# Kernel optimization log

Hardware: AMD Instinct MI355X
Metric: run time of the kernel (lower is better)

Reference implementation:

```python
import jax, jax.numpy as jnp
import numpy as np

TEMPERATURE = 0.1
EPS = 1e-8


def setup_inputs() -> dict:
    key = jax.random.key(0)
    k1, k2 = jax.random.split(key)
    N, D = 4096, 512
    features = jax.random.normal(k1, (N, D), dtype=jnp.float32)
    labels = jax.random.randint(k2, (N,), 0, 100, dtype=jnp.int64)
    return {"features": features, "labels": labels}


def reference(features, labels):
    # FFT along feature dim -> complex (N, D)
    cf = jnp.fft.fft(features)
    N = cf.shape[0]

    # All-pairs complex dot product expressed as a GEMM:
    # Re(sum_d u_d * conj(v_d)) for every (anchor, contrast) pair -> (N, N)
    dot_real = jnp.real(cf @ jnp.conj(cf).T)

    # L2 norm of complex vectors: sqrt(sum |cf|^2) -> (N,)
    norms = jnp.linalg.norm(cf, axis=-1)

    sim = dot_real / (norms[:, None] * norms[None, :])  # cosine sim (N, N)
    sim = sim / TEMPERATURE

    # Positive-pair mask (same label), excluding the diagonal (self)
    same_label = (labels[:, None] == labels[None, :]).astype(sim.dtype)
    logits_mask = 1.0 - jnp.eye(N, dtype=sim.dtype)
    mask = same_label * logits_mask

    # Faithful to the original: exp without max-subtraction (sim bounded by 1/tau)
    exp_logits = jnp.exp(sim) * logits_mask
    log_prob = sim - jnp.log(exp_logits.sum(axis=1, keepdims=True))

    mean_log_prob_pos = (mask * log_prob).sum(axis=1) / (mask.sum(axis=1) + EPS)
    return -mean_log_prob_pos.mean()
```

## Files before the change

kernel.cpp:

```cpp
#include <hip/hip_runtime.h>
#include <hip/hip_bf16.h>
#include <math.h>


#define NROWS 4096
#define DDIM  512
#define BM    128
#define BN    128
#define BK    32
#define NB    32
#define NTRI  (NB * (NB + 1) / 2)

typedef __attribute__((ext_vector_type(8))) short  short8;
typedef __attribute__((ext_vector_type(4))) float  floatx4;

__device__ inline unsigned short f2bf(float x) {
    unsigned u = __float_as_uint(x);
    return (unsigned short)((u + 0x7FFFu + ((u >> 16) & 1u)) >> 16);
}

__device__ inline float dpp_add16(float v) {
    v += __int_as_float(__builtin_amdgcn_update_dpp(
        0, __float_as_int(v), 0xB1, 0xF, 0xF, true));
    v += __int_as_float(__builtin_amdgcn_update_dpp(
        0, __float_as_int(v), 0x4E, 0xF, 0xF, true));
    v += __int_as_float(__builtin_amdgcn_update_dpp(
        0, __float_as_int(v), 0x141, 0xF, 0xF, true));
    v += __int_as_float(__builtin_amdgcn_update_dpp(
        0, __float_as_int(v), 0x140, 0xF, 0xF, true));
    return v;
}

__global__ __launch_bounds__(256) void prep_kernel(
    const float* __restrict__ F, const int* __restrict__ labels,
    unsigned short* __restrict__ Fb, float* __restrict__ invn,
    float* __restrict__ S, float* __restrict__ P, int* __restrict__ hist) {
    const int wave = threadIdx.x >> 6, lane = threadIdx.x & 63;
    const int row = blockIdx.x * 4 + wave;
    const float4* p = (const float4*)(F + (size_t)row * DDIM);
    float4 v0 = p[lane];
    float4 v1 = p[lane + 64];
    float s = v0.x * v0.x + v0.y * v0.y + v0.z * v0.z + v0.w * v0.w
            + v1.x * v1.x + v1.y * v1.y + v1.z * v1.z + v1.w * v1.w;
    ushort4 o0 = { f2bf(v0.x), f2bf(v0.y), f2bf(v0.z), f2bf(v0.w) };
    ushort4 o1 = { f2bf(v1.x), f2bf(v1.y), f2bf(v1.z), f2bf(v1.w) };
    ushort4* q = (ushort4*)(Fb + (size_t)row * DDIM);
    q[lane] = o0;
    q[lane + 64] = o1;
#pragma unroll
    for (int m = 1; m < 64; m <<= 1) s += __shfl_xor(s, m, 64);
    if (lane == 0) {
        invn[row] = rsqrtf(s) * 3.16227766017f;
        S[row] = 0.f;
        P[row] = 0.f;
    }
    if (blockIdx.x == 0) {
        __shared__ int h[128];
        if (threadIdx.x < 128) h[threadIdx.x] = 0;
        __syncthreads();
        for (int i = threadIdx.x; i < NROWS; i += 256)
            atomicAdd(&h[labels[i]], 1);
        __syncthreads();
        if (threadIdx.x < 128) hist[threadIdx.x] = h[threadIdx.x];
    }
}

__global__ __launch_bounds__(256) void fused_sym_kernel(
    const unsigned short* __restrict__ Fb, const float* __restrict__ invn,
    const int* __restrict__ labels,
    float* __restrict__ S, float* __restrict__ P) {
    __shared__ unsigned short As[BM * BK];
    __shared__ unsigned short Bs[BN * BK];

    int t = blockIdx.x;
    int bi = (int)((65.0f - sqrtf(65.0f * 65.0f - 8.0f * (float)t)) * 0.5f);
    while (bi > 0 && bi * NB - bi * (bi - 1) / 2 > t) --bi;
    while ((bi + 1) * NB - (bi + 1) * bi / 2 <= t) ++bi;
    const int bj = bi + (t - (bi * NB - bi * (bi - 1) / 2));
    const bool diag = (bi == bj);
    const int ib = bi * BM, jb = bj * BN;

    const int tid = threadIdx.x;
    const int wave = tid >> 6;
    const int lane = tid & 63;
    const int wx = wave & 1;
    const int wy = wave >> 1;
    const int lrow = lane & 15;
    const int lquad = lane >> 4;

    floatx4 acc[4][4];
#pragma unroll
    for (int mi = 0; mi < 4; ++mi)
#pragma unroll
        for (int ni = 0; ni < 4; ++ni) acc[mi][ni] = (floatx4){0.f, 0.f, 0.f, 0.f};

    for (int k0 = 0; k0 < DDIM; k0 += BK) {
        __syncthreads();
        int u = tid;
#pragma unroll
        for (int c = 0; c < 2; ++c, u += 256) {
            const unsigned short* ga =
                Fb + (size_t)(ib + (u >> 2)) * DDIM + k0 + (u & 3) * 8;
            const unsigned short* gb =
                Fb + (size_t)(jb + (u >> 2)) * DDIM + k0 + (u & 3) * 8;
            __builtin_amdgcn_global_load_lds(
                (const __attribute__((address_space(1))) unsigned int*)ga,
                (__attribute__((address_space(3))) unsigned int*)(As + u * 8),
                16, 0, 0);
            __builtin_amdgcn_global_load_lds(
                (const __attribute__((address_space(1))) unsigned int*)gb,
                (__attribute__((address_space(3))) unsigned int*)(Bs + u * 8),
                16, 0, 0);
        }
        __syncthreads();

        short8 a[4], b[4];
#pragma unroll
        for (int mi = 0; mi < 4; ++mi)
            a[mi] = *(const short8*)(As + (wy * 64 + mi * 16 + lrow) * BK + lquad * 8);
#pragma unroll
        for (int ni = 0; ni < 4; ++ni)
            b[ni] = *(const short8*)(Bs + (wx * 64 + ni * 16 + lrow) * BK + lquad * 8);
#pragma unroll
        for (int mi = 0; mi < 4; ++mi)
#pragma unroll
            for (int ni = 0; ni < 4; ++ni)
                acc[mi][ni] = __builtin_amdgcn_mfma_f32_16x16x32_bf16(
                    a[mi], b[ni], acc[mi][ni], 0, 0, 0);
    }

    float inB[4];
    int lB[4];
#pragma unroll
    for (int ni = 0; ni < 4; ++ni) {
        int j = jb + wx * 64 + ni * 16 + lrow;
        inB[ni] = invn[j];
        lB[ni] = labels[j];
    }
    float inA[4][4];
    int lA[4][4];
#pragma unroll
    for (int mi = 0; mi < 4; ++mi)
#pragma unroll
        for (int r = 0; r < 4; ++r) {
            int i = ib + wy * 64 + mi * 16 + lquad * 4 + r;
            inA[mi][r] = invn[i];
            lA[mi][r] = labels[i];
        }

    float ecol[4] = {0.f, 0.f, 0.f, 0.f};
    float pcol[4] = {0.f, 0.f, 0.f, 0.f};

#pragma unroll
    for (int mi = 0; mi < 4; ++mi) {
#pragma unroll
        for (int r = 0; r < 4; ++r) {
            const int i = ib + wy * 64 + mi * 16 + lquad * 4 + r;
            float es = 0.f, ps = 0.f;
#pragma unroll
            for (int ni = 0; ni < 4; ++ni) {
                const int j = jb + wx * 64 + ni * 16 + lrow;
                float sim = acc[mi][ni][r] * inA[mi][r] * inB[ni];
                float e = __expf(sim);
                float pm = (lA[mi][r] == lB[ni]) ? sim : 0.f;
                if (diag && i == j) { e = 0.f; pm = 0.f; }
                es += e; ps += pm;
                ecol[ni] += e; pcol[ni] += pm;
            }
            es = dpp_add16(es);
            ps = dpp_add16(ps);
            if (lrow == 0) {
                atomicAdd(&S[i], es);
                atomicAdd(&P[i], ps);
            }
        }
    }

    if (!diag) {
#pragma unroll
        for (int ni = 0; ni < 4; ++ni) {
            float e = ecol[ni], pq = pcol[ni];
            e += __shfl_xor(e, 16, 64);
            e += __shfl_xor(e, 32, 64);
            pq += __shfl_xor(pq, 16, 64);
            pq += __shfl_xor(pq, 32, 64);
            if (lquad == 0) {
                int j = jb + wx * 64 + ni * 16 + lrow;
                atomicAdd(&S[j], e);
                atomicAdd(&P[j], pq);
            }
        }
    }
}

__global__ __launch_bounds__(1024) void final_kernel(
    const float* __restrict__ S, const float* __restrict__ P,
    const int* __restrict__ labels, const int* __restrict__ hist,
    float* __restrict__ out) {
    float local = 0.f;
    for (int i = threadIdx.x; i < NROWS; i += 1024) {
        float cnt = (float)(hist[labels[i]] - 1);
        local += (P[i] - cnt * logf(S[i])) / (cnt + 1e-8f);
    }
#pragma unroll
    for (int m = 1; m < 64; m <<= 1) local += __shfl_xor(local, m, 64);
    __shared__ float red[16];
    int wave = threadIdx.x >> 6;
    if ((threadIdx.x & 63) == 0) red[wave] = local;
    __syncthreads();
    if (threadIdx.x == 0) {
        float s = 0.f;
#pragma unroll
        for (int w = 0; w < 16; ++w) s += red[w];
        out[0] = -s / (float)NROWS;
    }
}

extern "C" void kernel_launch(void* const* d_in, const int* in_sizes, int n_in,
                              void* d_out, int out_size, void* d_ws, size_t ws_size,
                              hipStream_t stream) {
    const float* F = (const float*)d_in[0];
    const int* labels = (const int*)d_in[1];
    float* out = (float*)d_out;

    float* invn = (float*)d_ws;
    float* S = invn + NROWS;
    float* P = S + NROWS;
    int* hist = (int*)(P + NROWS);
    unsigned short* Fb = (unsigned short*)(hist + 128);

    prep_kernel<<<dim3(NROWS / 4), dim3(256), 0, stream>>>(
        F, labels, Fb, invn, S, P, hist);
    fused_sym_kernel<<<dim3(NTRI), dim3(256), 0, stream>>>(
        Fb, invn, labels, S, P);
    final_kernel<<<dim3(1), dim3(1024), 0, stream>>>(S, P, labels, hist, out);
}
```

Measured before the change: 95.46 us.

## Replace LDS-staged 128x128 tiles with per-wave 64x64 direct-from-global register tiles

Each wave now owns its own 64x64 triangular tile and loads bf16 operands straight from global memory into registers with double buffering, dropping shared memory and block-wide barriers. This removes __syncthreads stalls and LDS traffic but loses operand sharing between waves, so global/L2 traffic roughly doubles. The grid holds 4x more tiles (2080 waves in 520 blocks), giving more parallelism and more atomics in the epilogue.

```diff
diff --git a/kernel.cpp b/kernel.cpp
--- a/kernel.cpp
+++ b/kernel.cpp
@@ -5,11 +5,9 @@
 
 #define NROWS 4096
 #define DDIM  512
-#define BM    128
-#define BN    128
-#define BK    32
-#define NB    32
-#define NTRI  (NB * (NB + 1) / 2)
+#define TW    64
+#define NBG   (NROWS / TW)
+#define NTRI  (NBG * (NBG + 1) / 2)
 
 typedef __attribute__((ext_vector_type(8))) short  short8;
 typedef __attribute__((ext_vector_type(4))) float  floatx4;
@@ -65,75 +63,64 @@
     }
 }
 
-__global__ __launch_bounds__(256) void fused_sym_kernel(
+__global__ __launch_bounds__(256) void fused_direct_kernel(
     const unsigned short* __restrict__ Fb, const float* __restrict__ invn,
     const int* __restrict__ labels,
     float* __restrict__ S, float* __restrict__ P) {
-    __shared__ unsigned short As[BM * BK];
-    __shared__ unsigned short Bs[BN * BK];
-
-    int t = blockIdx.x;
-    int bi = (int)((65.0f - sqrtf(65.0f * 65.0f - 8.0f * (float)t)) * 0.5f);
-    while (bi > 0 && bi * NB - bi * (bi - 1) / 2 > t) --bi;
-    while ((bi + 1) * NB - (bi + 1) * bi / 2 <= t) ++bi;
-    const int bj = bi + (t - (bi * NB - bi * (bi - 1) / 2));
-    const bool diag = (bi == bj);
-    const int ib = bi * BM, jb = bj * BN;
-
-    const int tid = threadIdx.x;
-    const int wave = tid >> 6;
-    const int lane = tid & 63;
-    const int wx = wave & 1;
-    const int wy = wave >> 1;
+    const int wid = blockIdx.x * 4 + (threadIdx.x >> 6);
+    const int lane = threadIdx.x & 63;
     const int lrow = lane & 15;
     const int lquad = lane >> 4;
 
+    int bi = (int)((129.0f - sqrtf(16641.0f - 8.0f * (float)wid)) * 0.5f);
+    while (bi > 0 && bi * NBG - bi * (bi - 1) / 2 > wid) --bi;
+    while ((bi + 1) * NBG - (bi + 1) * bi / 2 <= wid) ++bi;
+    const int bj = bi + (wid - (bi * NBG - bi * (bi - 1) / 2));
+    const bool diag = (bi == bj);
+    const int ib = bi * TW, jb = bj * TW;
+
+    const unsigned short* baseA = Fb + (size_t)(ib + lrow) * DDIM + lquad * 8;
+    const unsigned short* baseB = Fb + (size_t)(jb + lrow) * DDIM + lquad * 8;
+
     floatx4 acc[4][4];
 #pragma unroll
     for (int mi = 0; mi < 4; ++mi)
 #pragma unroll
         for (int ni = 0; ni < 4; ++ni) acc[mi][ni] = (floatx4){0.f, 0.f, 0.f, 0.f};
 
-    for (int k0 = 0; k0 < DDIM; k0 += BK) {
-        __syncthreads();
-        int u = tid;
-#pragma unroll
-        for (int c = 0; c < 2; ++c, u += 256) {
-            const unsigned short* ga =
-                Fb + (size_t)(ib + (u >> 2)) * DDIM + k0 + (u & 3) * 8;
-            const unsigned short* gb =
-                Fb + (size_t)(jb + (u >> 2)) * DDIM + k0 + (u & 3) * 8;
-            __builtin_amdgcn_global_load_lds(
-                (const __attribute__((address_space(1))) unsigned int*)ga,
-                (__attribute__((address_space(3))) unsigned int*)(As + u * 8),
-                16, 0, 0);
-            __builtin_amdgcn_global_load_lds(
-                (const __attribute__((address_space(1))) unsigned int*)gb,
-                (__attribute__((address_space(3))) unsigned int*)(Bs + u * 8),
-                16, 0, 0);
-        }
-        __syncthreads();
-
-        short8 a[4], b[4];
-#pragma unroll
-        for (int mi = 0; mi < 4; ++mi)
-            a[mi] = *(const short8*)(As + (wy * 64 + mi * 16 + lrow) * BK + lquad * 8);
-#pragma unroll
-        for (int ni = 0; ni < 4; ++ni)
-            b[ni] = *(const short8*)(Bs + (wx * 64 + ni * 16 + lrow) * BK + lquad * 8);
+    short8 af[2][4], bf[2][4];
+#pragma unroll
+    for (int mi = 0; mi < 4; ++mi)
+        af[0][mi] = *(const short8*)(baseA + (size_t)mi * 16 * DDIM);
+#pragma unroll
+    for (int ni = 0; ni < 4; ++ni)
+        bf[0][ni] = *(const short8*)(baseB + (size_t)ni * 16 * DDIM);
+
+#pragma unroll
+    for (int ks = 0; ks < 16; ++ks) {
+        const int cur = ks & 1, nxt = cur ^ 1;
+        if (ks < 15) {
+            const int ko = (ks + 1) * 32;
+#pragma unroll
+            for (int mi = 0; mi < 4; ++mi)
+                af[nxt][mi] = *(const short8*)(baseA + (size_t)mi * 16 * DDIM + ko);
+#pragma unroll
+            for (int ni = 0; ni < 4; ++ni)
+                bf[nxt][ni] = *(const short8*)(baseB + (size_t)ni * 16 * DDIM + ko);
+        }
 #pragma unroll
         for (int mi = 0; mi < 4; ++mi)
 #pragma unroll
             for (int ni = 0; ni < 4; ++ni)
                 acc[mi][ni] = __builtin_amdgcn_mfma_f32_16x16x32_bf16(
-                    a[mi], b[ni], acc[mi][ni], 0, 0, 0);
+                    af[cur][mi], bf[cur][ni], acc[mi][ni], 0, 0, 0);
     }
 
     float inB[4];
     int lB[4];
 #pragma unroll
     for (int ni = 0; ni < 4; ++ni) {
-        int j = jb + wx * 64 + ni * 16 + lrow;
+        int j = jb + ni * 16 + lrow;
         inB[ni] = invn[j];
         lB[ni] = labels[j];
     }
@@ -143,7 +130,7 @@
     for (int mi = 0; mi < 4; ++mi)
 #pragma unroll
         for (int r = 0; r < 4; ++r) {
-            int i = ib + wy * 64 + mi * 16 + lquad * 4 + r;
+            int i = ib + mi * 16 + lquad * 4 + r;
             inA[mi][r] = invn[i];
             lA[mi][r] = labels[i];
         }
@@ -155,11 +142,11 @@
     for (int mi = 0; mi < 4; ++mi) {
 #pragma unroll
         for (int r = 0; r < 4; ++r) {
-            const int i = ib + wy * 64 + mi * 16 + lquad * 4 + r;
+            const int i = ib + mi * 16 + lquad * 4 + r;
             float es = 0.f, ps = 0.f;
 #pragma unroll
             for (int ni = 0; ni < 4; ++ni) {
-                const int j = jb + wx * 64 + ni * 16 + lrow;
+                const int j = jb + ni * 16 + lrow;
                 float sim = acc[mi][ni][r] * inA[mi][r] * inB[ni];
                 float e = __expf(sim);
                 float pm = (lA[mi][r] == lB[ni]) ? sim : 0.f;
@@ -185,7 +172,7 @@
             pq += __shfl_xor(pq, 16, 64);
             pq += __shfl_xor(pq, 32, 64);
             if (lquad == 0) {
-                int j = jb + wx * 64 + ni * 16 + lrow;
+                int j = jb + ni * 16 + lrow;
                 atomicAdd(&S[j], e);
                 atomicAdd(&P[j], pq);
             }
@@ -231,7 +218,7 @@
 
     prep_kernel<<<dim3(NROWS / 4), dim3(256), 0, stream>>>(
         F, labels, Fb, invn, S, P, hist);
-    fused_sym_kernel<<<dim3(NTRI), dim3(256), 0, stream>>>(
+    fused_direct_kernel<<<dim3(NTRI / 4), dim3(256), 0, stream>>>(
         Fb, invn, labels, S, P);
     final_kernel<<<dim3(1), dim3(1024), 0, stream>>>(S, P, labels, hist, out);
 }
```

Result: slower. 120.3 us (+26.0%).
